# Optimization experiments

Measured on AMD Instinct MI355X. Metric: run time of the kernel, lower is better.

The kernel has to match this reference:

```python
import jax, jax.numpy as jnp
import numpy as np

B, NP, NJ, ND = 16, 64, 15, 128
SIGMA = 15.0        # cfg.MULTI_PERSON.POSE_SIGMA
BIG = 1.0e5         # sentinel used to mask padded reference persons
EPS = 1e-8


def setup_inputs() -> dict:
    key = jax.random.key(0)
    k1, k2, k3, k4, k5 = jax.random.split(key, 5)
    # 3D plane-sweep hypotheses in the reference camera frame (z>0 so projection is safe)
    uv = jax.random.uniform(k1, (B, NP, NJ, ND, 2), minval=-0.5, maxval=0.5)
    z = jax.random.uniform(k2, (B, NP, NJ, ND, 1), minval=2.0, maxval=10.0)
    poses_3d = jnp.concatenate([uv * z, z], axis=-1).astype(jnp.float32)
    # detected 2D poses in the reference view, pixel coordinates
    poses_2d_ref = (jax.random.uniform(k3, (B, NP, NJ, 2)) * jnp.array([1920.0, 1080.0], jnp.float32)).astype(jnp.float32)
    vis_ref = (jax.random.uniform(k4, (B, NP, NJ)) < 0.8).astype(jnp.float32)
    num_persons_ref = jax.random.randint(k5, (B,), 1, NP + 1).astype(jnp.int32)
    R = jnp.tile(jnp.eye(3, dtype=jnp.float32), (B, 1, 1))
    T = jnp.zeros((B, 3), jnp.float32)
    f = jnp.full((B, 2), 1000.0, jnp.float32)
    c = jnp.tile(jnp.array([960.0, 540.0], jnp.float32), (B, 1))
    image_w = jnp.full((B,), 1920.0, jnp.float32)
    image_h = jnp.full((B,), 1080.0, jnp.float32)
    return dict(poses_3d=poses_3d, poses_2d_ref=poses_2d_ref, vis_ref=vis_ref,
                num_persons_ref=num_persons_ref, R=R, T=T, f=f, c=c,
                image_w=image_w, image_h=image_h)


def _project(pts, R, T, f, c):
    # pinhole projection: x_cam = R (X - T); 2d = f * xy/z + c
    xc = jnp.einsum('bij,bpkdj->bpkdi', R, pts - T[:, None, None, None, :])
    z = xc[..., 2:3]
    return f[:, None, None, None, :] * xc[..., :2] / z + c[:, None, None, None, :]


def reference(poses_3d, poses_2d_ref, vis_ref, num_persons_ref, R, T, f, c, image_w, image_h):
    # 1) project 3D hypotheses to the reference view -> [B,NP,NJ,ND,2]
    p2t = _project(poses_3d, R, T, f, c)
    # 2) visibility-weighted mean pairwise squared distance, expanded as
    #    |a|^2 + |b|^2 - 2 a.b to avoid the [B,NP,NP,NJ,ND,2] intermediate
    pt2 = jnp.sum(p2t ** 2, axis=-1)                      # [B,NP,NJ,ND]
    pr2 = jnp.sum(poses_2d_ref ** 2, axis=-1)             # [B,NQ,NJ]
    wpr = poses_2d_ref * vis_ref[..., None]               # [B,NQ,NJ,2]
    term1 = jnp.einsum('bpjd,bqj->bpqd', pt2, vis_ref)
    term2 = jnp.sum(pr2 * vis_ref, axis=-1)               # [B,NQ]
    term3 = jnp.einsum('bpjdc,bqjc->bpqd', p2t, wpr)
    vsum = jnp.sum(vis_ref, axis=-1)                      # [B,NQ]
    dist = (term1 + term2[:, None, :, None] - 2.0 * term3) / (vsum[:, None, :, None] + EPS)
    # 3) mask padded reference persons, nearest-pose matching
    valid = jnp.arange(NP)[None, :] < num_persons_ref[:, None]   # [B,NQ]
    dist = jnp.where(valid[:, None, :, None], dist, BIG)
    mm = jnp.argmin(dist, axis=2)                          # [B,NP,ND]
    # 4) gather matched 2D poses / visibilities
    b_idx = jnp.arange(B)[:, None, None]
    matched = jnp.transpose(poses_2d_ref[b_idx, mm], (0, 1, 3, 2, 4))  # [B,NP,NJ,ND,2]
    mvis = jnp.transpose(vis_ref[b_idx, mm], (0, 1, 3, 2))             # [B,NP,NJ,ND]
    # 5) exp score (non-panoptic branch) and in-image bounding
    mdist = jnp.sum((p2t - matched) ** 2, axis=-1)
    score = jnp.exp(-mdist / (SIGMA ** 2))
    iw = image_w[:, None, None, None]
    ih = image_h[:, None, None, None]
    inb = ((p2t[..., 0] >= 0) & (p2t[..., 1] >= 0) &
           (p2t[..., 0] <= iw - 1) & (p2t[..., 1] <= ih - 1)).astype(score.dtype)
    bounding = inb * mvis
    return score * bounding
```

## Files before the change

### kernel.cpp

```cpp
#include <hip/hip_runtime.h>

#define NPERS 64
#define NJOINT 15
#define NDEPTH 128
#define BIGF 100000.0f
#define EPSF 1e-8f
#define INFF 3.0e38f

#define F4E(v, e) ((e) == 0 ? (v).x : (e) == 1 ? (v).y : (e) == 2 ? (v).z : (v).w)

__global__
__attribute__((amdgpu_flat_work_group_size(256, 256)))
__attribute__((amdgpu_waves_per_eu(2, 2)))
void pose_match_kernel(
    const float* __restrict__ poses_3d,
    const float* __restrict__ p2d,
    const float* __restrict__ vis,
    const int*   __restrict__ nper,
    const float* __restrict__ Rm,
    const float* __restrict__ Tm,
    const float* __restrict__ fm,
    const float* __restrict__ cm,
    const float* __restrict__ iw_,
    const float* __restrict__ ih_,
    float* __restrict__ out)
{
    const int b    = blockIdx.x >> 6;
    const int rem  = blockIdx.x & 63;
    const int pp   = rem >> 1;
    const int dh   = rem & 1;
    const int p0   = pp * 2;
    const int tid  = threadIdx.x;
    const int wv   = tid >> 6;
    const int lane = tid & 63;
    const int d    = dh * 64 + lane;

    __shared__ float4 sq[NPERS][NJOINT];
    __shared__ float4 sco[NPERS][13];
    __shared__ float  bvred[4][2][64];
    __shared__ int    bqred[4][2][64];

    for (int i = tid; i < NPERS * NJOINT; i += 256) {
        int q = i / NJOINT, j = i % NJOINT;
        float v  = vis[(b * NPERS + q) * NJOINT + j];
        float rx = p2d[((b * NPERS + q) * NJOINT + j) * 2 + 0];
        float ry = p2d[((b * NPERS + q) * NJOINT + j) * 2 + 1];
        sq[q][j] = make_float4(v, rx, ry, 0.0f);
    }
    __syncthreads();

    if (tid < NPERS) {
        const int q = tid;
        float vs = 0.0f, t2 = 0.0f;
        #pragma unroll
        for (int j = 0; j < NJOINT; ++j) {
            float4 s = sq[q][j];
            vs += s.x;
            t2 = fmaf(s.y * s.y + s.z * s.z, s.x, t2);
        }
        float inv = 1.0f / (vs + EPSF);
        float o[48];
        #pragma unroll
        for (int j = 0; j < NJOINT; ++j) {
            float4 s = sq[q][j];
            o[j]      = s.x * inv;
            o[16 + j] = 2.0f * s.x * s.y * inv;
            o[32 + j] = 2.0f * s.x * s.z * inv;
        }
        o[15] = t2 * inv;
        o[31] = 0.0f;
        o[47] = 0.0f;
        #pragma unroll
        for (int k = 0; k < 12; ++k)
            sco[q][k] = make_float4(o[4*k], o[4*k+1], o[4*k+2], o[4*k+3]);
    }
    __syncthreads();

    const float R00 = Rm[b*9+0], R01 = Rm[b*9+1], R02 = Rm[b*9+2];
    const float R10 = Rm[b*9+3], R11 = Rm[b*9+4], R12 = Rm[b*9+5];
    const float R20 = Rm[b*9+6], R21 = Rm[b*9+7], R22 = Rm[b*9+8];
    const float T0 = Tm[b*3+0], T1 = Tm[b*3+1], T2 = Tm[b*3+2];
    const float fx = fm[b*2+0], fy = fm[b*2+1];
    const float cx = cm[b*2+0], cy = cm[b*2+1];
    const float iwm1 = iw_[b] - 1.0f;
    const float ihm1 = ih_[b] - 1.0f;
    const int   npv  = nper[b];

    float X0[NJOINT], Y0[NJOINT], X1[NJOINT], Y1[NJOINT];
    #pragma unroll
    for (int j = 0; j < NJOINT; ++j) {
        int base = (((b * NPERS + p0) * NJOINT + j) * NDEPTH + d) * 3;
        float a0 = poses_3d[base + 0] - T0;
        float a1 = poses_3d[base + 1] - T1;
        float a2 = poses_3d[base + 2] - T2;
        float xc0 = R00 * a0 + R01 * a1 + R02 * a2;
        float xc1 = R10 * a0 + R11 * a1 + R12 * a2;
        float xc2 = R20 * a0 + R21 * a1 + R22 * a2;
        float r   = __builtin_amdgcn_rcpf(xc2);
        X0[j] = fmaf(fx * xc0, r, cx);
        Y0[j] = fmaf(fy * xc1, r, cy);
    }
    #pragma unroll
    for (int j = 0; j < NJOINT; ++j) {
        int base = (((b * NPERS + p0 + 1) * NJOINT + j) * NDEPTH + d) * 3;
        float a0 = poses_3d[base + 0] - T0;
        float a1 = poses_3d[base + 1] - T1;
        float a2 = poses_3d[base + 2] - T2;
        float xc0 = R00 * a0 + R01 * a1 + R02 * a2;
        float xc1 = R10 * a0 + R11 * a1 + R12 * a2;
        float xc2 = R20 * a0 + R21 * a1 + R22 * a2;
        float r   = __builtin_amdgcn_rcpf(xc2);
        X1[j] = fmaf(fx * xc0, r, cx);
        Y1[j] = fmaf(fy * xc1, r, cy);
    }

    float bv0, bv1;
    int   bq0, bq1;
    if (npv < NPERS) { bv0 = bv1 = BIGF; bq0 = bq1 = npv; }
    else             { bv0 = bv1 = INFF; bq0 = bq1 = 0;   }

    for (int q = wv; q < npv; q += 4) {
        const float c = sco[q][3].w;
        float a0 = c, a1 = c;
        #pragma unroll
        for (int k = 0; k < 4; ++k) {
            float4 cw4 = sco[q][k];
            float4 cx4 = sco[q][4 + k];
            float4 cy4 = sco[q][8 + k];
            #pragma unroll
            for (int e = 0; e < 4; ++e) {
                if (k == 3 && e == 3) continue;
                const int j = k * 4 + e;
                float w  = F4E(cw4, e);
                float wx = F4E(cx4, e);
                float wy = F4E(cy4, e);
                float u;
                u = fmaf(w, X0[j], -wx); a0 = fmaf(X0[j], u, a0);
                u = fmaf(w, Y0[j], -wy); a0 = fmaf(Y0[j], u, a0);
                u = fmaf(w, X1[j], -wx); a1 = fmaf(X1[j], u, a1);
                u = fmaf(w, Y1[j], -wy); a1 = fmaf(Y1[j], u, a1);
            }
        }
        if (a0 < bv0) { bv0 = a0; bq0 = q; }
        if (a1 < bv1) { bv1 = a1; bq1 = q; }
    }
    bvred[wv][0][lane] = bv0;  bqred[wv][0][lane] = bq0;
    bvred[wv][1][lane] = bv1;  bqred[wv][1][lane] = bq1;
    __syncthreads();

#define EPILOGUE(PI, XA, YA)                                                  \
    if (wv == PI) {                                                           \
        float bestv = bvred[0][PI][lane];                                     \
        int   bestq = bqred[0][PI][lane];                                     \
        _Pragma("unroll")                                                     \
        for (int k = 1; k < 4; ++k) {                                         \
            float v  = bvred[k][PI][lane];                                    \
            int   qq = bqred[k][PI][lane];                                    \
            if (v < bestv || (v == bestv && qq < bestq)) {                    \
                bestv = v; bestq = qq;                                        \
            }                                                                 \
        }                                                                     \
        const int obase = ((b * NPERS + p0 + PI) * NJOINT) * NDEPTH + d;      \
        _Pragma("unroll")                                                     \
        for (int j = 0; j < NJOINT; ++j) {                                    \
            float4 v = sq[bestq][j];                                          \
            float xx = XA[j], yy = YA[j];                                     \
            float dx = xx - v.y;                                              \
            float dy = yy - v.z;                                              \
            float md = fmaf(dx, dx, dy * dy);                                 \
            float sc = __expf(-md * (1.0f / 225.0f));                         \
            float inb = (xx >= 0.0f && yy >= 0.0f &&                          \
                         xx <= iwm1 && yy <= ihm1) ? 1.0f : 0.0f;             \
            out[obase + j * NDEPTH] = sc * inb * v.x;                         \
        }                                                                     \
    }

    EPILOGUE(0, X0, Y0)
    EPILOGUE(1, X1, Y1)
#undef EPILOGUE
}

extern "C" void kernel_launch(void* const* d_in, const int* in_sizes, int n_in,
                              void* d_out, int out_size, void* d_ws, size_t ws_size,
                              hipStream_t stream) {
    const float* poses_3d = (const float*)d_in[0];
    const float* p2d      = (const float*)d_in[1];
    const float* vis      = (const float*)d_in[2];
    const int*   nper     = (const int*)d_in[3];
    const float* Rm       = (const float*)d_in[4];
    const float* Tm       = (const float*)d_in[5];
    const float* fm       = (const float*)d_in[6];
    const float* cm       = (const float*)d_in[7];
    const float* iw       = (const float*)d_in[8];
    const float* ih       = (const float*)d_in[9];
    float* out = (float*)d_out;

    const int B = in_sizes[3];
    dim3 grid(B * 64);
    dim3 block(256);
    pose_match_kernel<<<grid, block, 0, stream>>>(
        poses_3d, p2d, vis, nper, Rm, Tm, fm, cm, iw, ih, out);
}
```

Before: 26.96 us.

## Split reference persons across 8 waves with joint-streamed projection and accumulators

Raises the block to 512 threads so each of 8 waves owns a fixed slice of 8 reference persons. Each wave streams joints in groups of four, projecting them on the fly while accumulating distances for all 8 candidates in registers, instead of holding all 60 projected coordinates live. The epilogue re-reads and re-projects the 3D points rather than keeping them in registers. Every wave now loads and projects the full hypothesis set, which multiplies global reads and projection math in exchange for lower register pressure, higher occupancy and no serial loop over reference persons. Waves whose slice is empty skip the accumulation.

Result: slower. 58.89 us (+118.4%).

```diff
diff --git a/kernel.cpp b/kernel.cpp
--- a/kernel.cpp
+++ b/kernel.cpp
@@ -9,9 +9,7 @@
 
 #define F4E(v, e) ((e) == 0 ? (v).x : (e) == 1 ? (v).y : (e) == 2 ? (v).z : (v).w)
 
-__global__
-__attribute__((amdgpu_flat_work_group_size(256, 256)))
-__attribute__((amdgpu_waves_per_eu(2, 2)))
+__global__ __launch_bounds__(512, 8)
 void pose_match_kernel(
     const float* __restrict__ poses_3d,
     const float* __restrict__ p2d,
@@ -31,16 +29,16 @@
     const int dh   = rem & 1;
     const int p0   = pp * 2;
     const int tid  = threadIdx.x;
-    const int wv   = tid >> 6;
     const int lane = tid & 63;
     const int d    = dh * 64 + lane;
+    const int wvs  = __builtin_amdgcn_readfirstlane(tid >> 6);
 
     __shared__ float4 sq[NPERS][NJOINT];
     __shared__ float4 sco[NPERS][13];
-    __shared__ float  bvred[4][2][64];
-    __shared__ int    bqred[4][2][64];
-
-    for (int i = tid; i < NPERS * NJOINT; i += 256) {
+    __shared__ float  bvred[8][2][64];
+    __shared__ int    bqred[8][2][64];
+
+    for (int i = tid; i < NPERS * NJOINT; i += 512) {
         int q = i / NJOINT, j = i % NJOINT;
         float v  = vis[(b * NPERS + q) * NJOINT + j];
         float rx = p2d[((b * NPERS + q) * NJOINT + j) * 2 + 0];
@@ -86,74 +84,113 @@
     const float ihm1 = ih_[b] - 1.0f;
     const int   npv  = nper[b];
 
-    float X0[NJOINT], Y0[NJOINT], X1[NJOINT], Y1[NJOINT];
+    const int q0  = wvs * 8;
+    const int nvs = __builtin_amdgcn_readfirstlane(
+                        min(max(npv - q0, 0), 8));
+
+    const float* pA = poses_3d +
+        ((size_t)(b * NPERS + p0    ) * NJOINT * NDEPTH + d) * 3;
+    const float* pB = poses_3d +
+        ((size_t)(b * NPERS + p0 + 1) * NJOINT * NDEPTH + d) * 3;
+
+    float acc0[8], acc1[8];
     #pragma unroll
-    for (int j = 0; j < NJOINT; ++j) {
-        int base = (((b * NPERS + p0) * NJOINT + j) * NDEPTH + d) * 3;
-        float a0 = poses_3d[base + 0] - T0;
-        float a1 = poses_3d[base + 1] - T1;
-        float a2 = poses_3d[base + 2] - T2;
-        float xc0 = R00 * a0 + R01 * a1 + R02 * a2;
-        float xc1 = R10 * a0 + R11 * a1 + R12 * a2;
-        float xc2 = R20 * a0 + R21 * a1 + R22 * a2;
-        float r   = __builtin_amdgcn_rcpf(xc2);
-        X0[j] = fmaf(fx * xc0, r, cx);
-        Y0[j] = fmaf(fy * xc1, r, cy);
-    }
-    #pragma unroll
-    for (int j = 0; j < NJOINT; ++j) {
-        int base = (((b * NPERS + p0 + 1) * NJOINT + j) * NDEPTH + d) * 3;
-        float a0 = poses_3d[base + 0] - T0;
-        float a1 = poses_3d[base + 1] - T1;
-        float a2 = poses_3d[base + 2] - T2;
-        float xc0 = R00 * a0 + R01 * a1 + R02 * a2;
-        float xc1 = R10 * a0 + R11 * a1 + R12 * a2;
-        float xc2 = R20 * a0 + R21 * a1 + R22 * a2;
-        float r   = __builtin_amdgcn_rcpf(xc2);
-        X1[j] = fmaf(fx * xc0, r, cx);
-        Y1[j] = fmaf(fy * xc1, r, cy);
-    }
+    for (int k = 0; k < 8; ++k) {
+        float ct = sco[q0 + k][3].w;
+        acc0[k] = ct;
+        acc1[k] = ct;
+    }
+
+#define PASS(J0, NJP, KW)                                                     \
+    {                                                                         \
+        float XA[4], YA[4], XB[4], YB[4];                                     \
+        _Pragma("unroll")                                                     \
+        for (int jj = 0; jj < NJP; ++jj) {                                    \
+            const int off = (J0 + jj) * NDEPTH * 3;                           \
+            {                                                                 \
+                float a0 = pA[off + 0] - T0;                                  \
+                float a1 = pA[off + 1] - T1;                                  \
+                float a2 = pA[off + 2] - T2;                                  \
+                float xc0 = R00 * a0 + R01 * a1 + R02 * a2;                   \
+                float xc1 = R10 * a0 + R11 * a1 + R12 * a2;                   \
+                float xc2 = R20 * a0 + R21 * a1 + R22 * a2;                   \
+                float r   = __builtin_amdgcn_rcpf(xc2);                       \
+                XA[jj] = fmaf(fx * xc0, r, cx);                               \
+                YA[jj] = fmaf(fy * xc1, r, cy);                               \
+            }                                                                 \
+            {                                                                 \
+                float a0 = pB[off + 0] - T0;                                  \
+                float a1 = pB[off + 1] - T1;                                  \
+                float a2 = pB[off + 2] - T2;                                  \
+                float xc0 = R00 * a0 + R01 * a1 + R02 * a2;                   \
+                float xc1 = R10 * a0 + R11 * a1 + R12 * a2;                   \
+                float xc2 = R20 * a0 + R21 * a1 + R22 * a2;                   \
+                float r   = __builtin_amdgcn_rcpf(xc2);                       \
+                XB[jj] = fmaf(fx * xc0, r, cx);                               \
+                YB[jj] = fmaf(fy * xc1, r, cy);                               \
+            }                                                                 \
+        }                                                                     \
+        _Pragma("unroll")                                                     \
+        for (int g = 0; g < 2; ++g) {                                         \
+            if (g * 4 < nvs) {                     \
+                _Pragma("unroll")                                             \
+                for (int e = 0; e < 4; ++e) {                                 \
+                    const int kk = g * 4 + e;                                 \
+                    const int q  = q0 + kk;                                   \
+                    float4 w4 = sco[q][KW];                                   \
+                    float4 x4 = sco[q][4 + KW];                               \
+                    float4 y4 = sco[q][8 + KW];                               \
+                    _Pragma("unroll")                                         \
+                    for (int jj = 0; jj < NJP; ++jj) {                        \
+                        float w  = F4E(w4, jj);                               \
+                        float wx = F4E(x4, jj);                               \
+                        float wy = F4E(y4, jj);                               \
+                        float u;                                              \
+                        u = fmaf(w, XA[jj], -wx);                             \
+                        acc0[kk] = fmaf(XA[jj], u, acc0[kk]);                 \
+                        u = fmaf(w, YA[jj], -wy);                             \
+                        acc0[kk] = fmaf(YA[jj], u, acc0[kk]);                 \
+                        u = fmaf(w, XB[jj], -wx);                             \
+                        acc1[kk] = fmaf(XB[jj], u, acc1[kk]);                 \
+                        u = fmaf(w, YB[jj], -wy);                             \
+                        acc1[kk] = fmaf(YB[jj], u, acc1[kk]);                 \
+                    }                                                         \
+                }                                                             \
+            }                                                                 \
+        }                                                                     \
+    }
+
+    if (nvs > 0) {
+        PASS(0,  4, 0)
+        PASS(4,  4, 1)
+        PASS(8,  4, 2)
+        PASS(12, 3, 3)
+    }
+#undef PASS
 
     float bv0, bv1;
     int   bq0, bq1;
     if (npv < NPERS) { bv0 = bv1 = BIGF; bq0 = bq1 = npv; }
     else             { bv0 = bv1 = INFF; bq0 = bq1 = 0;   }
-
-    for (int q = wv; q < npv; q += 4) {
-        const float c = sco[q][3].w;
-        float a0 = c, a1 = c;
-        #pragma unroll
-        for (int k = 0; k < 4; ++k) {
-            float4 cw4 = sco[q][k];
-            float4 cx4 = sco[q][4 + k];
-            float4 cy4 = sco[q][8 + k];
-            #pragma unroll
-            for (int e = 0; e < 4; ++e) {
-                if (k == 3 && e == 3) continue;
-                const int j = k * 4 + e;
-                float w  = F4E(cw4, e);
-                float wx = F4E(cx4, e);
-                float wy = F4E(cy4, e);
-                float u;
-                u = fmaf(w, X0[j], -wx); a0 = fmaf(X0[j], u, a0);
-                u = fmaf(w, Y0[j], -wy); a0 = fmaf(Y0[j], u, a0);
-                u = fmaf(w, X1[j], -wx); a1 = fmaf(X1[j], u, a1);
-                u = fmaf(w, Y1[j], -wy); a1 = fmaf(Y1[j], u, a1);
-            }
+    #pragma unroll
+    for (int k = 0; k < 8; ++k) {
+        if (k < nvs) {
+            float d0 = acc0[k];
+            float d1 = acc1[k];
+            if (d0 < bv0) { bv0 = d0; bq0 = q0 + k; }
+            if (d1 < bv1) { bv1 = d1; bq1 = q0 + k; }
         }
-        if (a0 < bv0) { bv0 = a0; bq0 = q; }
-        if (a1 < bv1) { bv1 = a1; bq1 = q; }
-    }
-    bvred[wv][0][lane] = bv0;  bqred[wv][0][lane] = bq0;
-    bvred[wv][1][lane] = bv1;  bqred[wv][1][lane] = bq1;
+    }
+    bvred[wvs][0][lane] = bv0;  bqred[wvs][0][lane] = bq0;
+    bvred[wvs][1][lane] = bv1;  bqred[wvs][1][lane] = bq1;
     __syncthreads();
 
-#define EPILOGUE(PI, XA, YA)                                                  \
-    if (wv == PI) {                                                           \
+#define EPILOGUE(PI, PPTR)                                                    \
+    if (wvs == PI) {                                                          \
         float bestv = bvred[0][PI][lane];                                     \
         int   bestq = bqred[0][PI][lane];                                     \
         _Pragma("unroll")                                                     \
-        for (int k = 1; k < 4; ++k) {                                         \
+        for (int k = 1; k < 8; ++k) {                                         \
             float v  = bvred[k][PI][lane];                                    \
             int   qq = bqred[k][PI][lane];                                    \
             if (v < bestv || (v == bestv && qq < bestq)) {                    \
@@ -163,8 +200,17 @@
         const int obase = ((b * NPERS + p0 + PI) * NJOINT) * NDEPTH + d;      \
         _Pragma("unroll")                                                     \
         for (int j = 0; j < NJOINT; ++j) {                                    \
+            const int off = j * NDEPTH * 3;                                   \
+            float a0 = PPTR[off + 0] - T0;                                    \
+            float a1 = PPTR[off + 1] - T1;                                    \
+            float a2 = PPTR[off + 2] - T2;                                    \
+            float xc0 = R00 * a0 + R01 * a1 + R02 * a2;                       \
+            float xc1 = R10 * a0 + R11 * a1 + R12 * a2;                       \
+            float xc2 = R20 * a0 + R21 * a1 + R22 * a2;                       \
+            float r   = __builtin_amdgcn_rcpf(xc2);                           \
+            float xx  = fmaf(fx * xc0, r, cx);                                \
+            float yy  = fmaf(fy * xc1, r, cy);                                \
             float4 v = sq[bestq][j];                                          \
-            float xx = XA[j], yy = YA[j];                                     \
             float dx = xx - v.y;                                              \
             float dy = yy - v.z;                                              \
             float md = fmaf(dx, dx, dy * dy);                                 \
@@ -175,8 +221,8 @@
         }                                                                     \
     }
 
-    EPILOGUE(0, X0, Y0)
-    EPILOGUE(1, X1, Y1)
+    EPILOGUE(0, pA)
+    EPILOGUE(1, pB)
 #undef EPILOGUE
 }
 
@@ -197,7 +243,7 @@
 
     const int B = in_sizes[3];
     dim3 grid(B * 64);
-    dim3 block(256);
+    dim3 block(512);
     pose_match_kernel<<<grid, block, 0, stream>>>(
         poses_3d, p2d, vis, nper, Rm, Tm, fm, cm, iw, ih, out);
 }
```
